# Kernel optimization log

Measured on AMD Instinct MI355X. Metric: run time of the kernel, lower is better.

Reference implementation:

```python
import jax, jax.numpy as jnp
import numpy as np

EPS = 1e-7
NUM_NODES = 50000


def setup_inputs() -> dict:
    key = jax.random.key(0)
    k1, k2, k3 = jax.random.split(key, 3)
    n_nodes, n_edges, d = NUM_NODES, 800000, 64
    x = jax.random.normal(k1, (n_nodes, d), dtype=jnp.float32)
    edge_index = jax.random.randint(k2, (2, n_edges), 0, n_nodes, dtype=jnp.int64)
    W = jax.random.normal(k3, (d, d), dtype=jnp.float32) * (1.0 / np.sqrt(d))
    b = jnp.zeros((d,), dtype=jnp.float32)
    beta = jnp.ones((1,), dtype=jnp.float32)
    return {"x": x, "edge_index": edge_index, "W": W, "b": b, "beta": beta}


def _segment_softmax(logits, seg, num_segments):
    # numerically stable softmax over edges grouped by destination node, per channel
    m = jax.ops.segment_max(logits, seg, num_segments=num_segments)  # [N, d]
    m = jnp.where(jnp.isfinite(m), m, 0.0)  # empty segments -> -inf; neutralize
    e = jnp.exp(logits - m[seg])                                      # [E, d]
    denom = jax.ops.segment_sum(e, seg, num_segments=num_segments)    # [N, d]
    return e / (denom[seg] + 1e-16)


def reference(x, edge_index, W, b, beta):
    num_nodes, dim = x.shape
    dst = edge_index[0]
    src = edge_index[1]
    # gather + message encoder (ReLU) + eps
    edge_msg = jax.nn.relu(x[src]) + EPS                               # [E, d]
    # softmax_sg: softmax(beta * msg) per destination segment, beta is a stop-grad scalar
    alpha = _segment_softmax(beta[0] * edge_msg, dst, num_nodes)       # [E, d]
    h = edge_msg * alpha                                               # [E, d]
    # scatter-add aggregation to destination nodes
    agg = jax.ops.segment_sum(h, dst, num_segments=num_nodes)          # [N, d]
    # final dense linear (nn.Linear): agg @ W.T + b
    return agg @ W.T + b
```

## Files before the change

kernel.cpp:

```cpp
#include <hip/hip_runtime.h>
#include <hip/hip_fp16.h>

#define EPS 1e-7f

__global__ __launch_bounds__(512)
void binprep_kernel(const int* __restrict__ dst,
                    const int* __restrict__ src, int E, int cap,
                    const float* __restrict__ x, int M,
                    int* __restrict__ ccur,
                    unsigned* __restrict__ packed,
                    unsigned short* __restrict__ tm,
                    int binBlocks) {
    if ((int)blockIdx.x < binBlocks) {
        __shared__ int lc[256];
        __shared__ int lbase[256];
        int tid = threadIdx.x;
        if (tid < 256) lc[tid] = 0;
        __syncthreads();
        int e0 = blockIdx.x * 2048;
        int bb[4], rr[4];
        unsigned pk[4];
        #pragma unroll
        for (int i = 0; i < 4; ++i) {
            int e = e0 + i * 512 + tid;
            bb[i] = 0; rr[i] = 0; pk[i] = 0;
            if (e < E) {
                int d = dst[e];
                bb[i] = d >> 8;
                pk[i] = ((unsigned)(d & 255) << 16) | (unsigned)src[e];
                rr[i] = atomicAdd(&lc[bb[i]], 1);
            }
        }
        __syncthreads();
        if (tid < 256) {
            int c = lc[tid];
            if (c) lbase[tid] = tid * cap + atomicAdd(&ccur[tid], c);
        }
        __syncthreads();
        #pragma unroll
        for (int i = 0; i < 4; ++i) {
            int e = e0 + i * 512 + tid;
            if (e < E) packed[lbase[bb[i]] + rr[i]] = pk[i];
        }
    } else {
        int blk = blockIdx.x - binBlocks;
        int tid = threadIdx.x;
        const unsigned short sent = __half_as_ushort(__float2half_rn(-32.f));
        #pragma unroll
        for (int p = 0; p < 4; ++p) {
            int i = blk * 8192 + p * 2048 + tid * 4;
            if (i < M) {
                float4 v = *(const float4*)&x[i];
                ushort4 o;
                o.x = __half_as_ushort(__float2half_rn(fmaxf(v.x, 0.f) + EPS));
                o.y = __half_as_ushort(__float2half_rn(fmaxf(v.y, 0.f) + EPS));
                o.z = __half_as_ushort(__float2half_rn(fmaxf(v.z, 0.f) + EPS));
                o.w = __half_as_ushort(__float2half_rn(fmaxf(v.w, 0.f) + EPS));
                *(ushort4*)&tm[i] = o;
            } else if (i < M + 64) {
                ushort4 o; o.x = o.y = o.z = o.w = sent;
                *(ushort4*)&tm[i] = o;
            }
        }
    }
}

__global__ __launch_bounds__(512)
void fine_kernel(const unsigned* __restrict__ packed,
                 const int* __restrict__ ccur, int cap,
                 int2* __restrict__ nse,
                 unsigned short* __restrict__ sorted_src, int N) {
    __shared__ int lc[256];
    __shared__ int lcur[256];
    __shared__ int wsum[4];
    __shared__ unsigned stage_pk[6656];
    __shared__ unsigned short stage16[6656];
    int tid = threadIdx.x, b = blockIdx.x;
    int rs = b * cap;
    int len = ccur[b];
    if (tid < 256) lc[tid] = 0;
    __syncthreads();
    for (int i = tid; i < len; i += 512) {
        unsigned u = packed[rs + i];
        stage_pk[i] = u;
        atomicAdd(&lc[u >> 16], 1);
    }
    __syncthreads();
    if (tid < 256) {
        int lane = tid & 63, wid = tid >> 6;
        int incl = lc[tid];
        #pragma unroll
        for (int d = 1; d < 64; d <<= 1) {
            int t = __shfl_up(incl, d, 64);
            if (lane >= d) incl += t;
        }
        lcur[tid] = incl;
        if (lane == 63) wsum[wid] = incl;
    }
    __syncthreads();
    if (tid < 256) {
        int wid = tid >> 6;
        int base = 0;
        for (int w = 0; w < wid; ++w) base += wsum[w];
        int v = lc[tid];
        int excl = base + lcur[tid] - v;
        lcur[tid] = excl;
        int node = b * 256 + tid;
        if (node < N) nse[node] = make_int2(rs + excl, rs + excl + v);
    }
    __syncthreads();
    for (int i = tid; i < len; i += 512) {
        unsigned u = stage_pk[i];
        int pos = atomicAdd(&lcur[u >> 16], 1);
        stage16[pos] = (unsigned short)(u & 0xffffu);
    }
    __syncthreads();
    unsigned* dst32 = (unsigned*)&sorted_src[rs];
    int len2 = (len + 1) >> 1;
    for (int i = tid; i < len2; i += 512) {
        unsigned lo = stage16[2 * i];
        unsigned hi = (2 * i + 1 < len) ? (unsigned)stage16[2 * i + 1] : 0u;
        dst32[i] = lo | (hi << 16);
    }
}

__device__ __forceinline__ void acc2(unsigned w, float bt,
                                     float& s1a, float& s2a,
                                     float& s1b, float& s2b) {
    float m0 = __half2float(__ushort_as_half((unsigned short)(w & 0xffffu)));
    float m1 = __half2float(__ushort_as_half((unsigned short)(w >> 16)));
    float e0 = __expf(bt * m0);
    float e1 = __expf(bt * m1);
    s1a += e0; s2a = fmaf(m0, e0, s2a);
    s1b += e1; s2b = fmaf(m1, e1, s2b);
}

__global__ __launch_bounds__(512)
void node_kernel(const unsigned short* __restrict__ tm,
                 const int2* __restrict__ nse,
                 const unsigned short* __restrict__ sorted_src,
                 const float* __restrict__ W,
                 const float* __restrict__ b,
                 const float* __restrict__ beta,
                 float* __restrict__ out, int N) {
    __shared__ float WtS[64 * 65];
    __shared__ float aggS[512];

    int tid = threadIdx.x;
    #pragma unroll
    for (int idx = tid * 4; idx < 64 * 64; idx += 512 * 4) {
        float4 w4 = *(const float4*)&W[idx];
        int j = idx >> 6, c = idx & 63;
        WtS[(c + 0) * 65 + j] = w4.x;
        WtS[(c + 1) * 65 + j] = w4.y;
        WtS[(c + 2) * 65 + j] = w4.z;
        WtS[(c + 3) * 65 + j] = w4.w;
    }
    __syncthreads();

    const float bt = beta[0];
    const int wave = tid >> 6;
    const int lane = tid & 63;
    const int quarter = lane >> 4;
    const int chb = (lane & 15) << 3;
    const float bias = b[lane];
    const int stride = gridDim.x * 8;
    const int sent_row = N << 7;
    const unsigned char* tmb = (const unsigned char*)tm;
    float* as = &aggS[wave * 64];

    for (int node = blockIdx.x * 8 + wave; node < N; node += stride) {
        int2 se = nse[node];
        int start = se.x, end = se.y;
        float s1c0 = 0.f, s1c1 = 0.f, s1c2 = 0.f, s1c3 = 0.f;
        float s2c0 = 0.f, s2c1 = 0.f, s2c2 = 0.f, s2c3 = 0.f;
        for (int bse = start; bse < end; bse += 64) {
            int cnt = end - bse;
            if (cnt > 64) cnt = 64;
            int row = (lane < cnt) ? ((int)sorted_src[bse + lane] << 7)
                                   : sent_row;
            int r0 = __shfl(row, quarter, 64);
            int r1 = __shfl(row, 4 + quarter, 64);
            uint2 u0 = *(const uint2*)(tmb + (r0 + chb));
            uint2 u1 = *(const uint2*)(tmb + (r1 + chb));
            int k = 0;
            while (k + 8 < cnt) {
                int n0 = __shfl(row, k + 8 + quarter, 64);
                int n1 = __shfl(row, k + 12 + quarter, 64);
                uint2 v0 = *(const uint2*)(tmb + (n0 + chb));
                uint2 v1 = *(const uint2*)(tmb + (n1 + chb));
                acc2(u0.x, bt, s1c0, s2c0, s1c1, s2c1);
                acc2(u0.y, bt, s1c2, s2c2, s1c3, s2c3);
                acc2(u1.x, bt, s1c0, s2c0, s1c1, s2c1);
                acc2(u1.y, bt, s1c2, s2c2, s1c3, s2c3);
                u0 = v0; u1 = v1;
                k += 8;
            }
            acc2(u0.x, bt, s1c0, s2c0, s1c1, s2c1);
            acc2(u0.y, bt, s1c2, s2c2, s1c3, s2c3);
            acc2(u1.x, bt, s1c0, s2c0, s1c1, s2c1);
            acc2(u1.y, bt, s1c2, s2c2, s1c3, s2c3);
        }
        #define RED(s) s += __shfl_xor(s, 16, 64); s += __shfl_xor(s, 32, 64)
        RED(s1c0); RED(s1c1); RED(s1c2); RED(s1c3);
        RED(s2c0); RED(s2c1); RED(s2c2); RED(s2c3);
        #undef RED
        float4 g;
        g.x = __fdividef(s2c0, s1c0 + 1e-16f);
        g.y = __fdividef(s2c1, s1c1 + 1e-16f);
        g.z = __fdividef(s2c2, s1c2 + 1e-16f);
        g.w = __fdividef(s2c3, s1c3 + 1e-16f);
        if (lane < 16) *(float4*)&as[(lane & 15) << 2] = g;
        float acc = bias;
        #pragma unroll
        for (int c = 0; c < 64; c += 4) {
            float4 a4 = *(const float4*)&as[c];
            acc = fmaf(a4.x, WtS[(c + 0) * 65 + lane], acc);
            acc = fmaf(a4.y, WtS[(c + 1) * 65 + lane], acc);
            acc = fmaf(a4.z, WtS[(c + 2) * 65 + lane], acc);
            acc = fmaf(a4.w, WtS[(c + 3) * 65 + lane], acc);
        }
        out[(size_t)node * 64 + lane] = acc;
    }
}

extern "C" void kernel_launch(void* const* d_in, const int* in_sizes, int n_in,
                              void* d_out, int out_size, void* d_ws, size_t ws_size,
                              hipStream_t stream) {
    const float* x    = (const float*)d_in[0];
    const int*   ei   = (const int*)d_in[1];
    const float* W    = (const float*)d_in[2];
    const float* b    = (const float*)d_in[3];
    const float* beta = (const float*)d_in[4];
    float* out = (float*)d_out;

    const int N = in_sizes[0] / 64;
    const int E = in_sizes[1] / 2;
    const int* dst = ei;
    const int* src = ei + E;
    const int NB = (N + 255) >> 8;
    const int M = N * 64;

    int cap = (E + NB - 1) / NB;
    cap = ((cap + cap / 2 + 256) + 255) & ~255;
    if (cap > 6656) cap = 6656;

    auto align = [](size_t v) { return (v + 255) & ~(size_t)255; };
    size_t off = 0;
    char* ws = (char*)d_ws;
    int2* nse   = (int2*)(ws + off);      off += align((size_t)N * 8);
    int* ccur   = (int*)(ws + off);       off += align((size_t)NB * 4);
    unsigned* packed = (unsigned*)(ws + off);
    off += align((size_t)NB * cap * 4);
    unsigned short* sorted_src = (unsigned short*)(ws + off);
    off += align((size_t)NB * cap * 2);
    unsigned short* tm = (unsigned short*)(ws + off);

    const int binBlocks  = (E + 2047) / 2048;
    const int prepBlocks = (M + 64 + 8191) / 8192;
    hipMemsetAsync(ccur, 0, (size_t)NB * 4, stream);
    binprep_kernel<<<binBlocks + prepBlocks, 512, 0, stream>>>(
        dst, src, E, cap, x, M, ccur, packed, tm, binBlocks);
    fine_kernel<<<NB, 512, 0, stream>>>(packed, ccur, cap, nse, sorted_src, N);

    int node_blocks = (N + 7) / 8;
    if (node_blocks > 1024) node_blocks = 1024;
    node_kernel<<<node_blocks, 512, 0, stream>>>(tm, nse, sorted_src,
                                                 W, b, beta, out, N);
}
```

Before: 139.6 us.

## Precompute per-node exp and msg*exp, split aggregation and linear into kernels

The prep stage now computes exp(beta*m) and m*exp(beta*m) once per source node and stores both as a packed fp16 pair, so the gather loop only sums values instead of evaluating an exp per edge per channel. The node kernel is remapped to one quarter-wave per destination node with 16-byte loads, and no longer needs a cross-quarter shuffle reduction. The dense linear moves into a separate kernel that reads an fp32 agg buffer from workspace. This doubles gathered bytes per edge and adds an extra kernel launch plus an N×64 round trip through memory. Storing exp values in fp16 risks overflow when beta*m is large.

Measured after the change: 133.6 us. 1.05x faster.

```diff
diff --git a/kernel.cpp b/kernel.cpp
--- a/kernel.cpp
+++ b/kernel.cpp
@@ -6,10 +6,11 @@
 __global__ __launch_bounds__(512)
 void binprep_kernel(const int* __restrict__ dst,
                     const int* __restrict__ src, int E, int cap,
-                    const float* __restrict__ x, int M,
+                    const float* __restrict__ x,
+                    const float* __restrict__ beta, int M,
                     int* __restrict__ ccur,
                     unsigned* __restrict__ packed,
-                    unsigned short* __restrict__ tm,
+                    unsigned* __restrict__ tp,
                     int binBlocks) {
     if ((int)blockIdx.x < binBlocks) {
         __shared__ int lc[256];
@@ -45,21 +46,30 @@
     } else {
         int blk = blockIdx.x - binBlocks;
         int tid = threadIdx.x;
-        const unsigned short sent = __half_as_ushort(__float2half_rn(-32.f));
+        const float bt = beta[0];
         #pragma unroll
         for (int p = 0; p < 4; ++p) {
             int i = blk * 8192 + p * 2048 + tid * 4;
             if (i < M) {
                 float4 v = *(const float4*)&x[i];
-                ushort4 o;
-                o.x = __half_as_ushort(__float2half_rn(fmaxf(v.x, 0.f) + EPS));
-                o.y = __half_as_ushort(__float2half_rn(fmaxf(v.y, 0.f) + EPS));
-                o.z = __half_as_ushort(__float2half_rn(fmaxf(v.z, 0.f) + EPS));
-                o.w = __half_as_ushort(__float2half_rn(fmaxf(v.w, 0.f) + EPS));
-                *(ushort4*)&tm[i] = o;
+                uint4 o;
+                float m, ex;
+                m = fmaxf(v.x, 0.f) + EPS; ex = __expf(bt * m);
+                o.x = (unsigned)__half_as_ushort(__float2half_rn(ex)) |
+                      ((unsigned)__half_as_ushort(__float2half_rn(m * ex)) << 16);
+                m = fmaxf(v.y, 0.f) + EPS; ex = __expf(bt * m);
+                o.y = (unsigned)__half_as_ushort(__float2half_rn(ex)) |
+                      ((unsigned)__half_as_ushort(__float2half_rn(m * ex)) << 16);
+                m = fmaxf(v.z, 0.f) + EPS; ex = __expf(bt * m);
+                o.z = (unsigned)__half_as_ushort(__float2half_rn(ex)) |
+                      ((unsigned)__half_as_ushort(__float2half_rn(m * ex)) << 16);
+                m = fmaxf(v.w, 0.f) + EPS; ex = __expf(bt * m);
+                o.w = (unsigned)__half_as_ushort(__float2half_rn(ex)) |
+                      ((unsigned)__half_as_ushort(__float2half_rn(m * ex)) << 16);
+                *(uint4*)&tp[i] = o;
             } else if (i < M + 64) {
-                ushort4 o; o.x = o.y = o.z = o.w = sent;
-                *(ushort4*)&tm[i] = o;
+                uint4 o; o.x = o.y = o.z = o.w = 0u;
+                *(uint4*)&tp[i] = o;
             }
         }
     }
@@ -124,31 +134,77 @@
     }
 }
 
-__device__ __forceinline__ void acc2(unsigned w, float bt,
-                                     float& s1a, float& s2a,
-                                     float& s1b, float& s2b) {
-    float m0 = __half2float(__ushort_as_half((unsigned short)(w & 0xffffu)));
-    float m1 = __half2float(__ushort_as_half((unsigned short)(w >> 16)));
-    float e0 = __expf(bt * m0);
-    float e1 = __expf(bt * m1);
-    s1a += e0; s2a = fmaf(m0, e0, s2a);
-    s1b += e1; s2b = fmaf(m1, e1, s2b);
-}
-
-__global__ __launch_bounds__(512)
-void node_kernel(const unsigned short* __restrict__ tm,
+__device__ __forceinline__ float f16lo(unsigned w) {
+    return __half2float(__ushort_as_half((unsigned short)(w & 0xffffu)));
+}
+__device__ __forceinline__ float f16hi(unsigned w) {
+    return __half2float(__ushort_as_half((unsigned short)(w >> 16)));
+}
+
+__global__ __launch_bounds__(256)
+void node_kernel(const unsigned* __restrict__ tp,
                  const int2* __restrict__ nse,
-                 const unsigned short* __restrict__ sorted_src,
-                 const float* __restrict__ W,
-                 const float* __restrict__ b,
-                 const float* __restrict__ beta,
-                 float* __restrict__ out, int N) {
+                 const unsigned short* __restrict__ ss,
+                 float* __restrict__ agg, int N) {
+    const int tid = threadIdx.x;
+    const int wave = tid >> 6;
+    const int lane = tid & 63;
+    const int quarter = lane >> 4;
+    const int l16 = lane & 15;
+    const int qbase = quarter << 4;
+    const int chb = l16 << 4;
+    const int sent = N << 8;
+    const unsigned char* tb = (const unsigned char*)tp;
+
+    const int node = blockIdx.x * 16 + wave * 4 + quarter;
+    int start = 0, cnt = 0;
+    if (node < N) { int2 se = nse[node]; start = se.x; cnt = se.y - se.x; }
+
+    float s1x = 0.f, s1y = 0.f, s1z = 0.f, s1w = 0.f;
+    float s2x = 0.f, s2y = 0.f, s2z = 0.f, s2w = 0.f;
+
+    for (int chunk = 0; chunk < cnt; chunk += 16) {
+        int rem = cnt - chunk;
+        if (rem > 16) rem = 16;
+        int row = (l16 < rem) ? ((int)ss[start + chunk + l16] << 8) : sent;
+        for (int k = 0; k < rem; k += 4) {
+            int r0 = __shfl(row, qbase + k + 0, 64);
+            int r1 = __shfl(row, qbase + k + 1, 64);
+            int r2 = __shfl(row, qbase + k + 2, 64);
+            int r3 = __shfl(row, qbase + k + 3, 64);
+            uint4 u0 = *(const uint4*)(tb + (r0 + chb));
+            uint4 u1 = *(const uint4*)(tb + (r1 + chb));
+            uint4 u2 = *(const uint4*)(tb + (r2 + chb));
+            uint4 u3 = *(const uint4*)(tb + (r3 + chb));
+            #define ACC(u) \
+                s1x += f16lo(u.x); s2x += f16hi(u.x); \
+                s1y += f16lo(u.y); s2y += f16hi(u.y); \
+                s1z += f16lo(u.z); s2z += f16hi(u.z); \
+                s1w += f16lo(u.w); s2w += f16hi(u.w)
+            ACC(u0); ACC(u1); ACC(u2); ACC(u3);
+            #undef ACC
+        }
+    }
+    if (node < N) {
+        float4 g;
+        g.x = __fdividef(s2x, s1x + 1e-16f);
+        g.y = __fdividef(s2y, s1y + 1e-16f);
+        g.z = __fdividef(s2z, s1z + 1e-16f);
+        g.w = __fdividef(s2w, s1w + 1e-16f);
+        *(float4*)&agg[((size_t)node << 6) + (l16 << 2)] = g;
+    }
+}
+
+__global__ __launch_bounds__(256)
+void linear_kernel(const float* __restrict__ agg,
+                   const float* __restrict__ W,
+                   const float* __restrict__ b,
+                   float* __restrict__ out, int N) {
     __shared__ float WtS[64 * 65];
-    __shared__ float aggS[512];
-
+    __shared__ float aggS[256];
     int tid = threadIdx.x;
     #pragma unroll
-    for (int idx = tid * 4; idx < 64 * 64; idx += 512 * 4) {
+    for (int idx = tid * 4; idx < 64 * 64; idx += 256 * 4) {
         float4 w4 = *(const float4*)&W[idx];
         int j = idx >> 6, c = idx & 63;
         WtS[(c + 0) * 65 + j] = w4.x;
@@ -157,60 +213,13 @@
         WtS[(c + 3) * 65 + j] = w4.w;
     }
     __syncthreads();
-
-    const float bt = beta[0];
     const int wave = tid >> 6;
     const int lane = tid & 63;
-    const int quarter = lane >> 4;
-    const int chb = (lane & 15) << 3;
     const float bias = b[lane];
-    const int stride = gridDim.x * 8;
-    const int sent_row = N << 7;
-    const unsigned char* tmb = (const unsigned char*)tm;
+    const int stride = gridDim.x * 4;
     float* as = &aggS[wave * 64];
-
-    for (int node = blockIdx.x * 8 + wave; node < N; node += stride) {
-        int2 se = nse[node];
-        int start = se.x, end = se.y;
-        float s1c0 = 0.f, s1c1 = 0.f, s1c2 = 0.f, s1c3 = 0.f;
-        float s2c0 = 0.f, s2c1 = 0.f, s2c2 = 0.f, s2c3 = 0.f;
-        for (int bse = start; bse < end; bse += 64) {
-            int cnt = end - bse;
-            if (cnt > 64) cnt = 64;
-            int row = (lane < cnt) ? ((int)sorted_src[bse + lane] << 7)
-                                   : sent_row;
-            int r0 = __shfl(row, quarter, 64);
-            int r1 = __shfl(row, 4 + quarter, 64);
-            uint2 u0 = *(const uint2*)(tmb + (r0 + chb));
-            uint2 u1 = *(const uint2*)(tmb + (r1 + chb));
-            int k = 0;
-            while (k + 8 < cnt) {
-                int n0 = __shfl(row, k + 8 + quarter, 64);
-                int n1 = __shfl(row, k + 12 + quarter, 64);
-                uint2 v0 = *(const uint2*)(tmb + (n0 + chb));
-                uint2 v1 = *(const uint2*)(tmb + (n1 + chb));
-                acc2(u0.x, bt, s1c0, s2c0, s1c1, s2c1);
-                acc2(u0.y, bt, s1c2, s2c2, s1c3, s2c3);
-                acc2(u1.x, bt, s1c0, s2c0, s1c1, s2c1);
-                acc2(u1.y, bt, s1c2, s2c2, s1c3, s2c3);
-                u0 = v0; u1 = v1;
-                k += 8;
-            }
-            acc2(u0.x, bt, s1c0, s2c0, s1c1, s2c1);
-            acc2(u0.y, bt, s1c2, s2c2, s1c3, s2c3);
-            acc2(u1.x, bt, s1c0, s2c0, s1c1, s2c1);
-            acc2(u1.y, bt, s1c2, s2c2, s1c3, s2c3);
-        }
-        #define RED(s) s += __shfl_xor(s, 16, 64); s += __shfl_xor(s, 32, 64)
-        RED(s1c0); RED(s1c1); RED(s1c2); RED(s1c3);
-        RED(s2c0); RED(s2c1); RED(s2c2); RED(s2c3);
-        #undef RED
-        float4 g;
-        g.x = __fdividef(s2c0, s1c0 + 1e-16f);
-        g.y = __fdividef(s2c1, s1c1 + 1e-16f);
-        g.z = __fdividef(s2c2, s1c2 + 1e-16f);
-        g.w = __fdividef(s2c3, s1c3 + 1e-16f);
-        if (lane < 16) *(float4*)&as[(lane & 15) << 2] = g;
+    for (int node = blockIdx.x * 4 + wave; node < N; node += stride) {
+        as[lane] = agg[(size_t)node * 64 + lane];
         float acc = bias;
         #pragma unroll
         for (int c = 0; c < 64; c += 4) {
@@ -254,17 +263,18 @@
     off += align((size_t)NB * cap * 4);
     unsigned short* sorted_src = (unsigned short*)(ws + off);
     off += align((size_t)NB * cap * 2);
-    unsigned short* tm = (unsigned short*)(ws + off);
+    unsigned* tp = (unsigned*)(ws + off); off += align(((size_t)N + 1) * 64 * 4);
+    float* agg  = (float*)(ws + off);     off += align((size_t)M * 4);
 
     const int binBlocks  = (E + 2047) / 2048;
     const int prepBlocks = (M + 64 + 8191) / 8192;
     hipMemsetAsync(ccur, 0, (size_t)NB * 4, stream);
     binprep_kernel<<<binBlocks + prepBlocks, 512, 0, stream>>>(
-        dst, src, E, cap, x, M, ccur, packed, tm, binBlocks);
+        dst, src, E, cap, x, beta, M, ccur, packed, tp, binBlocks);
     fine_kernel<<<NB, 512, 0, stream>>>(packed, ccur, cap, nse, sorted_src, N);
-
-    int node_blocks = (N + 7) / 8;
-    if (node_blocks > 1024) node_blocks = 1024;
-    node_kernel<<<node_blocks, 512, 0, stream>>>(tm, nse, sorted_src,
-                                                 W, b, beta, out, N);
-}
+    node_kernel<<<(N + 15) / 16, 256, 0, stream>>>(tp, nse, sorted_src, agg, N);
+
+    int lin_blocks = (N + 3) / 4;
+    if (lin_blocks > 2048) lin_blocks = 2048;
+    linear_kernel<<<lin_blocks, 256, 0, stream>>>(agg, W, b, out, N);
+}
```
